# Performance work log

Measured on AMD Instinct MI355X. Metric: run time of the kernel, lower is better.

## Reference

```python
import jax, jax.numpy as jnp
import numpy as np
import math

HIDDEN = 1024
HEADS = 16
LAYERS = 4
IN_DIM = 512
OUT_DIM = 1024
B, S = 4, 2048


def _pos_encoding(seq_len, dim):
    pos = jnp.arange(seq_len, dtype=jnp.float32)[:, None]            # [S,1]
    div = jnp.exp(jnp.arange(0, dim, 2, dtype=jnp.float32) * (-math.log(10000.0) / dim))  # [D/2]
    ang = pos * div                                                   # [S,D/2]
    # interleave: even idx sin, odd idx cos
    return jnp.stack([jnp.sin(ang), jnp.cos(ang)], axis=-1).reshape(seq_len, dim)


def _layernorm(x, g, b, eps=1e-5):
    mu = jnp.mean(x, axis=-1, keepdims=True)
    var = jnp.var(x, axis=-1, keepdims=True)
    return (x - mu) * jax.lax.rsqrt(var + eps) * g + b


def setup_inputs() -> dict:
    key = jax.random.key(0)
    ks = jax.random.split(key, 8)
    d = {
        'x': jax.random.normal(ks[0], (B, S, IN_DIM), jnp.float32),
        'in_W': jax.random.normal(ks[1], (IN_DIM, HIDDEN), jnp.float32) * (1.0 / math.sqrt(IN_DIM)),
        'in_b': jnp.zeros((HIDDEN,), jnp.float32),
        'qkv_W': jax.random.normal(ks[2], (LAYERS, HIDDEN, 3 * HIDDEN), jnp.float32) * (1.0 / math.sqrt(HIDDEN)),
        'qkv_b': jnp.zeros((LAYERS, 3 * HIDDEN), jnp.float32),
        'out_W': jax.random.normal(ks[3], (LAYERS, HIDDEN, HIDDEN), jnp.float32) * (1.0 / math.sqrt(HIDDEN)),
        'out_b': jnp.zeros((LAYERS, HIDDEN), jnp.float32),
        'ln1_g': jnp.ones((LAYERS, HIDDEN), jnp.float32),
        'ln1_b': jnp.zeros((LAYERS, HIDDEN), jnp.float32),
        'ln2_g': jnp.ones((LAYERS, HIDDEN), jnp.float32),
        'ln2_b': jnp.zeros((LAYERS, HIDDEN), jnp.float32),
        'ff1_W': jax.random.normal(ks[4], (LAYERS, HIDDEN, 4 * HIDDEN), jnp.float32) * (1.0 / math.sqrt(HIDDEN)),
        'ff1_b': jnp.zeros((LAYERS, 4 * HIDDEN), jnp.float32),
        'ff2_W': jax.random.normal(ks[5], (LAYERS, 4 * HIDDEN, HIDDEN), jnp.float32) * (1.0 / math.sqrt(4 * HIDDEN)),
        'ff2_b': jnp.zeros((LAYERS, HIDDEN), jnp.float32),
        'fin_g': jnp.ones((HIDDEN,), jnp.float32),
        'fin_b': jnp.zeros((HIDDEN,), jnp.float32),
        'op_W': jax.random.normal(ks[6], (HIDDEN, OUT_DIM), jnp.float32) * (1.0 / math.sqrt(HIDDEN)),
        'op_b': jnp.zeros((OUT_DIM,), jnp.float32),
    }
    return d


def reference(x, in_W, in_b, qkv_W, qkv_b, out_W, out_b, ln1_g, ln1_b, ln2_g, ln2_b,
              ff1_W, ff1_b, ff2_W, ff2_b, fin_g, fin_b, op_W, op_b):
    b, s, _ = x.shape
    dh = HIDDEN // HEADS
    h = x @ in_W + in_b                                   # [B,S,D]
    h = h * math.sqrt(HIDDEN) + _pos_encoding(s, HIDDEN)  # scaled + PE (dropout=eval)
    for i in range(LAYERS):
        qkv = (h @ qkv_W[i] + qkv_b[i]).reshape(b, s, 3, HEADS, dh)
        q, k, v = qkv[:, :, 0], qkv[:, :, 1], qkv[:, :, 2]
        scores = jnp.einsum('bqhd,bkhd->bhqk', q, k) / math.sqrt(dh)
        attn = jax.nn.softmax(scores, axis=-1)
        ctx = jnp.einsum('bhqk,bkhd->bqhd', attn, v).reshape(b, s, HIDDEN)
        h = _layernorm(h + (ctx @ out_W[i] + out_b[i]), ln1_g[i], ln1_b[i])
        ff = jax.nn.relu(h @ ff1_W[i] + ff1_b[i]) @ ff2_W[i] + ff2_b[i]
        h = _layernorm(h + ff, ln2_g[i], ln2_b[i])
    h = _layernorm(h, fin_g, fin_b)
    return h @ op_W + op_b
```

## Files before the change

kernel.cpp:

```cpp
#include <hip/hip_runtime.h>
#include <math.h>

typedef unsigned short u16;
typedef __attribute__((ext_vector_type(8))) __bf16 bf16x8;
typedef __attribute__((ext_vector_type(4))) float floatx4;
typedef unsigned int __attribute__((address_space(1))) g_u32;
typedef unsigned int __attribute__((address_space(3))) l_u32;

#define EPI_BIAS  1
#define EPI_RELU  2
#define EPI_EMBED 8

__device__ __forceinline__ float bf2f(u16 u) {
    union { unsigned int i; float f; } v; v.i = ((unsigned int)u) << 16; return v.f;
}
__device__ __forceinline__ u16 f2bf(float f) {
    union { __bf16 b; u16 u; } v; v.b = (__bf16)f; return v.u;
}
__device__ __forceinline__ void gl_lds16(const void* g, void* l) {
    __builtin_amdgcn_global_load_lds((const g_u32*)g, (l_u32*)l, 16, 0, 0);
}
__device__ __forceinline__ float posenc(int s, int c) {
    double e = exp((double)(c & 1022) * (-9.210340371976184 / 1024.0));
    double ang = (double)s * e;
    return (float)((c & 1) ? cos(ang) : sin(ang));
}

template<bool SPLIT>
__global__ __launch_bounds__(256) void transpose_f2b(
    const float* __restrict__ in, u16* __restrict__ oh, u16* __restrict__ ol,
    int R, int C) {
    __shared__ float tile[32][33];
    int bx = blockIdx.x * 32, by = blockIdx.y * 32;
    int tx = threadIdx.x & 31, ty = threadIdx.x >> 5;
    #pragma unroll
    for (int i = ty; i < 32; i += 8) tile[i][tx] = in[(size_t)(by + i) * C + bx + tx];
    __syncthreads();
    #pragma unroll
    for (int i = ty; i < 32; i += 8) {
        float f = tile[tx][i];
        u16 hi = f2bf(f);
        oh[(size_t)(bx + i) * R + by + tx] = hi;
        if (SPLIT) ol[(size_t)(bx + i) * R + by + tx] = f2bf(f - bf2f(hi));
    }
}

template<int AMODE, int EPI, bool ACCUM, bool WF, bool WB>
__global__ __launch_bounds__(256) void gemm_k(
    const void* __restrict__ Ap, const u16* __restrict__ Bt,
    const float* __restrict__ bias,
    float* __restrict__ outF, u16* __restrict__ outB,
    int M, int N, int K) {
    __shared__ alignas(16) u16 As[128 * 32];
    __shared__ alignas(16) u16 Bs[128 * 32];
    const int tid = threadIdx.x;
    const int wave = tid >> 6, lane = tid & 63;
    const int l16 = lane & 15, quad = lane >> 4;
    const int bm = blockIdx.x * 128, bn = blockIdx.y * 128;
    const int wm = (wave & 1) * 64, wn = (wave >> 1) * 64;
    const int sr = tid >> 2, sc = (tid & 3) * 8;

    const u16* Abf = (const u16*)Ap;
    const float* Af = (const float*)Ap;

    floatx4 acc[4][4];
    floatx4 zero = {0.0f, 0.0f, 0.0f, 0.0f};
    #pragma unroll
    for (int i = 0; i < 4; ++i)
        #pragma unroll
        for (int j = 0; j < 4; ++j) acc[i][j] = zero;

    for (int k0 = 0; k0 < K; k0 += 32) {
        if (AMODE == 0) {
            #pragma unroll
            for (int p = 0; p < 2; ++p) {
                const u16* g = Abf + (size_t)(bm + sr + 64 * p) * K + k0 + sc;
                gl_lds16(g, &As[(p * 64 + (wave << 4)) * 32]);
            }
        } else {
            #pragma unroll
            for (int p = 0; p < 2; ++p) {
                const float* g = Af + (size_t)(bm + sr + 64 * p) * K + k0 + sc;
                union { u16 u[8]; uint4 v; } tmp;
                #pragma unroll
                for (int j = 0; j < 8; ++j) {
                    float f = g[j];
                    u16 h = f2bf(f);
                    if (AMODE == 2) h = f2bf(f - bf2f(h));
                    tmp.u[j] = h;
                }
                *(uint4*)&As[(sr + 64 * p) * 32 + sc] = tmp.v;
            }
        }
        #pragma unroll
        for (int p = 0; p < 2; ++p) {
            const u16* g = Bt + (size_t)(bn + sr + 64 * p) * K + k0 + sc;
            gl_lds16(g, &Bs[(p * 64 + (wave << 4)) * 32]);
        }
        __syncthreads();
        bf16x8 af[4], bfr[4];
        #pragma unroll
        for (int i = 0; i < 4; ++i) af[i] = *(const bf16x8*)&As[(wm + i * 16 + l16) * 32 + quad * 8];
        #pragma unroll
        for (int j = 0; j < 4; ++j) bfr[j] = *(const bf16x8*)&Bs[(wn + j * 16 + l16) * 32 + quad * 8];
        #pragma unroll
        for (int i = 0; i < 4; ++i)
            #pragma unroll
            for (int j = 0; j < 4; ++j)
                acc[i][j] = __builtin_amdgcn_mfma_f32_16x16x32_bf16(af[i], bfr[j], acc[i][j], 0, 0, 0);
        __syncthreads();
    }

    #pragma unroll
    for (int i = 0; i < 4; ++i) {
        #pragma unroll
        for (int r = 0; r < 4; ++r) {
            int row = bm + wm + i * 16 + quad * 4 + r;
            #pragma unroll
            for (int j = 0; j < 4; ++j) {
                int col = bn + wn + j * 16 + l16;
                float v = acc[i][j][r];
                if (EPI & EPI_BIAS) v += bias[col];
                if (ACCUM) v += outF[(size_t)row * N + col];
                if (EPI & EPI_EMBED) { v = v * 32.0f + posenc(row & 2047, col); }
                if (EPI & EPI_RELU) v = fmaxf(v, 0.0f);
                if (WF) outF[(size_t)row * N + col] = v;
                if (WB) outB[(size_t)row * N + col] = f2bf(v);
            }
        }
    }
}

__global__ __launch_bounds__(256) void attn_k(
    const float* __restrict__ qkv, u16* __restrict__ ctx) {
    constexpr int KSTR = 72;
    constexpr int VSTR = 72;
    constexpr int PSTR = 88;
    __shared__ alignas(16) u16 Kh[2][64 * KSTR];
    __shared__ alignas(16) u16 Kl[2][64 * KSTR];
    __shared__ alignas(16) u16 Vt[2][64 * VSTR];
    __shared__ alignas(16) u16 Ps[128 * PSTR];

    const int tid = threadIdx.x, wave = tid >> 6, lane = tid & 63;
    const int l16 = lane & 15, quad = lane >> 4;
    const int bh = blockIdx.x >> 4, qt = blockIdx.x & 15;
    const int b = bh >> 4, h = bh & 15;
    const size_t base = (size_t)b * 2048 * 3072;
    const int wq = wave * 32;

    const int kr = tid >> 2, kcb = (tid & 3) * 16;
    const float* gK = qkv + base + (size_t)kr * 3072 + 1024 + h * 64 + kcb;
    const int vk = lane, vdg = wave * 16;
    const float* gV = qkv + base + (size_t)vk * 3072 + 2048 + h * 64 + vdg;

    bf16x8 qh[2][2], ql[2][2];
    #pragma unroll
    for (int i = 0; i < 2; ++i) {
        const float* g = qkv + base + (size_t)(qt * 128 + wq + i * 16 + l16) * 3072 + h * 64 + quad * 8;
        #pragma unroll
        for (int kk = 0; kk < 2; ++kk) {
            float4 va = ((const float4*)(g + kk * 32))[0];
            float4 vb = ((const float4*)(g + kk * 32))[1];
            float f[8] = {va.x, va.y, va.z, va.w, vb.x, vb.y, vb.z, vb.w};
            union { u16 u[8]; bf16x8 v; } th, tl;
            #pragma unroll
            for (int j = 0; j < 8; ++j) {
                float s = f[j] * 0.125f;
                u16 hi = f2bf(s);
                th.u[j] = hi;
                tl.u[j] = f2bf(s - bf2f(hi));
            }
            qh[i][kk] = th.v; ql[i][kk] = tl.v;
        }
    }

    float4 pk4[4], pv4[4];
    auto LOAD = [&](int c) {
        const float* g = gK + (size_t)(c * 64) * 3072;
        pk4[0] = ((const float4*)g)[0]; pk4[1] = ((const float4*)g)[1];
        pk4[2] = ((const float4*)g)[2]; pk4[3] = ((const float4*)g)[3];
        const float* g2 = gV + (size_t)(c * 64) * 3072;
        pv4[0] = ((const float4*)g2)[0]; pv4[1] = ((const float4*)g2)[1];
        pv4[2] = ((const float4*)g2)[2]; pv4[3] = ((const float4*)g2)[3];
    };
    auto STORE = [&](int bu) {
        const float* pf = (const float*)pk4;
        union { u16 u[8]; uint4 q; } h0, h1, s0, s1;
        #pragma unroll
        for (int j = 0; j < 8; ++j) {
            float a = pf[j], c2 = pf[8 + j];
            u16 ah = f2bf(a); h0.u[j] = ah; s0.u[j] = f2bf(a - bf2f(ah));
            u16 ch = f2bf(c2); h1.u[j] = ch; s1.u[j] = f2bf(c2 - bf2f(ch));
        }
        *(uint4*)&Kh[bu][kr * KSTR + kcb]     = h0.q;
        *(uint4*)&Kh[bu][kr * KSTR + kcb + 8] = h1.q;
        *(uint4*)&Kl[bu][kr * KSTR + kcb]     = s0.q;
        *(uint4*)&Kl[bu][kr * KSTR + kcb + 8] = s1.q;
        const float* vf = (const float*)pv4;
        #pragma unroll
        for (int j = 0; j < 16; ++j)
            Vt[bu][(vdg + j) * VSTR + vk] = f2bf(vf[j]);
    };

    floatx4 acc_o[2][4];
    float mrun[2][4], lrun[2][4];
    floatx4 zf = {0.0f, 0.0f, 0.0f, 0.0f};
    #pragma unroll
    for (int i = 0; i < 2; ++i)
        #pragma unroll
        for (int j = 0; j < 4; ++j) acc_o[i][j] = zf;
    #pragma unroll
    for (int i = 0; i < 2; ++i)
        #pragma unroll
        for (int r = 0; r < 4; ++r) { mrun[i][r] = -1e30f; lrun[i][r] = 0.0f; }

    LOAD(0); STORE(0); LOAD(1);
    __syncthreads();

    for (int c = 0; c < 32; ++c) {
        const int cur = c & 1;

        floatx4 acc_s[2][4];
        #pragma unroll
        for (int i = 0; i < 2; ++i)
            #pragma unroll
            for (int j = 0; j < 4; ++j) acc_s[i][j] = zf;
        #pragma unroll
        for (int kk = 0; kk < 2; ++kk) {
            bf16x8 kbh[4], kbl[4];
            #pragma unroll
            for (int j = 0; j < 4; ++j) {
                kbh[j] = *(const bf16x8*)&Kh[cur][(j * 16 + l16) * KSTR + kk * 32 + quad * 8];
                kbl[j] = *(const bf16x8*)&Kl[cur][(j * 16 + l16) * KSTR + kk * 32 + quad * 8];
            }
            #pragma unroll
            for (int i = 0; i < 2; ++i)
                #pragma unroll
                for (int j = 0; j < 4; ++j) {
                    acc_s[i][j] = __builtin_amdgcn_mfma_f32_16x16x32_bf16(qh[i][kk], kbh[j], acc_s[i][j], 0, 0, 0);
                    acc_s[i][j] = __builtin_amdgcn_mfma_f32_16x16x32_bf16(ql[i][kk], kbh[j], acc_s[i][j], 0, 0, 0);
                    acc_s[i][j] = __builtin_amdgcn_mfma_f32_16x16x32_bf16(qh[i][kk], kbl[j], acc_s[i][j], 0, 0, 0);
                }
        }

        #pragma unroll
        for (int i = 0; i < 2; ++i) {
            #pragma unroll
            for (int r = 0; r < 4; ++r) {
                float mx = fmaxf(fmaxf(acc_s[i][0][r], acc_s[i][1][r]),
                                 fmaxf(acc_s[i][2][r], acc_s[i][3][r]));
                #pragma unroll
                for (int off = 8; off; off >>= 1) mx = fmaxf(mx, __shfl_xor(mx, off));
                float nm = fmaxf(mrun[i][r], mx);
                float sc = __expf(mrun[i][r] - nm);
                mrun[i][r] = nm;
                float rs = 0.0f;
                #pragma unroll
                for (int j = 0; j < 4; ++j) {
                    float p = __expf(acc_s[i][j][r] - nm);
                    acc_s[i][j][r] = p;
                    rs += p;
                }
                #pragma unroll
                for (int off = 8; off; off >>= 1) rs += __shfl_xor(rs, off);
                lrun[i][r] = lrun[i][r] * sc + rs;
                #pragma unroll
                for (int jd = 0; jd < 4; ++jd) acc_o[i][jd][r] *= sc;
                #pragma unroll
                for (int j = 0; j < 4; ++j)
                    Ps[(wq + i * 16 + quad * 4 + r) * PSTR + j * 16 + l16] = f2bf(acc_s[i][j][r]);
            }
        }
        asm volatile("s_waitcnt lgkmcnt(0)" ::: "memory");

        #pragma unroll
        for (int kk = 0; kk < 2; ++kk) {
            bf16x8 pa[2], vb[4];
            #pragma unroll
            for (int i = 0; i < 2; ++i)
                pa[i] = *(const bf16x8*)&Ps[(wq + i * 16 + l16) * PSTR + kk * 32 + quad * 8];
            #pragma unroll
            for (int jd = 0; jd < 4; ++jd)
                vb[jd] = *(const bf16x8*)&Vt[cur][(jd * 16 + l16) * VSTR + kk * 32 + quad * 8];
            #pragma unroll
            for (int i = 0; i < 2; ++i)
                #pragma unroll
                for (int jd = 0; jd < 4; ++jd)
                    acc_o[i][jd] = __builtin_amdgcn_mfma_f32_16x16x32_bf16(pa[i], vb[jd], acc_o[i][jd], 0, 0, 0);
        }

        if (c + 1 < 32) STORE(cur ^ 1);
        __syncthreads();
        if (c + 2 < 32) LOAD(c + 2);
    }

    #pragma unroll
    for (int i = 0; i < 2; ++i) {
        #pragma unroll
        for (int r = 0; r < 4; ++r) {
            float inv = 1.0f / lrun[i][r];
            size_t ro = (size_t)(b * 2048 + qt * 128 + wq + i * 16 + quad * 4 + r) * 1024 + h * 64;
            #pragma unroll
            for (int jd = 0; jd < 4; ++jd)
                ctx[ro + jd * 16 + l16] = f2bf(acc_o[i][jd][r] * inv);
        }
    }
}

__global__ __launch_bounds__(256) void ln_k(
    float* __restrict__ h, const float* __restrict__ g, const float* __restrict__ bb) {
    const int row = blockIdx.x, tid = threadIdx.x;
    const int wave = tid >> 6, lane = tid & 63;
    float4 v = *(const float4*)(h + (size_t)row * 1024 + tid * 4);
    float x[4] = {v.x, v.y, v.z, v.w};
    float s = x[0] + x[1] + x[2] + x[3];
    float s2 = x[0] * x[0] + x[1] * x[1] + x[2] * x[2] + x[3] * x[3];
    for (int off = 32; off; off >>= 1) { s += __shfl_xor(s, off); s2 += __shfl_xor(s2, off); }
    __shared__ float red[8];
    if (lane == 0) { red[wave] = s; red[4 + wave] = s2; }
    __syncthreads();
    s = red[0] + red[1] + red[2] + red[3];
    s2 = red[4] + red[5] + red[6] + red[7];
    float mu = s * (1.0f / 1024.0f);
    float var = s2 * (1.0f / 1024.0f) - mu * mu;
    float rs = rsqrtf(var + 1e-5f);
    float4 gg = *(const float4*)(g + tid * 4);
    float4 bp = *(const float4*)(bb + tid * 4);
    float4 o;
    o.x = (x[0] - mu) * rs * gg.x + bp.x;
    o.y = (x[1] - mu) * rs * gg.y + bp.y;
    o.z = (x[2] - mu) * rs * gg.z + bp.z;
    o.w = (x[3] - mu) * rs * gg.w + bp.w;
    *(float4*)(h + (size_t)row * 1024 + tid * 4) = o;
}

extern "C" void kernel_launch(void* const* d_in, const int* in_sizes, int n_in,
                              void* d_out, int out_size, void* d_ws, size_t ws_size,
                              hipStream_t stream) {
    const float* x     = (const float*)d_in[0];
    const float* in_W  = (const float*)d_in[1];
    const float* in_b  = (const float*)d_in[2];
    const float* qkv_W = (const float*)d_in[3];
    const float* qkv_b = (const float*)d_in[4];
    const float* out_W = (const float*)d_in[5];
    const float* out_b = (const float*)d_in[6];
    const float* ln1_g = (const float*)d_in[7];
    const float* ln1_b = (const float*)d_in[8];
    const float* ln2_g = (const float*)d_in[9];
    const float* ln2_b = (const float*)d_in[10];
    const float* ff1_W = (const float*)d_in[11];
    const float* ff1_b = (const float*)d_in[12];
    const float* ff2_W = (const float*)d_in[13];
    const float* ff2_b = (const float*)d_in[14];
    const float* fin_g = (const float*)d_in[15];
    const float* fin_b = (const float*)d_in[16];
    const float* op_W  = (const float*)d_in[17];
    const float* op_b  = (const float*)d_in[18];

    size_t off = 0;
    char* wsb = (char*)d_ws;
    auto alloc = [&](size_t bytes) { void* p = wsb + off; off += (bytes + 255) & ~(size_t)255; return p; };
    u16*   BtH  = (u16*)alloc((size_t)4096 * 1024 * 2);
    u16*   BtL  = (u16*)alloc((size_t)3072 * 1024 * 2);
    float* hbuf = (float*)alloc((size_t)8192 * 1024 * 4);
    float* qkvb = (float*)alloc((size_t)8192 * 3072 * 4);
    u16*   ctxb = (u16*)alloc((size_t)8192 * 1024 * 2);
    if (off > ws_size) return;

    dim3 tb(256);

    transpose_f2b<true><<<dim3(32, 16), tb, 0, stream>>>(in_W, BtH, BtL, 512, 1024);
    gemm_k<1, 0, false, true, false><<<dim3(64, 8), tb, 0, stream>>>(
        x, BtH, nullptr, hbuf, nullptr, 8192, 1024, 512);
    gemm_k<1, 0, true, true, false><<<dim3(64, 8), tb, 0, stream>>>(
        x, BtL, nullptr, hbuf, nullptr, 8192, 1024, 512);
    gemm_k<2, EPI_BIAS | EPI_EMBED, true, true, false><<<dim3(64, 8), tb, 0, stream>>>(
        x, BtH, in_b, hbuf, nullptr, 8192, 1024, 512);

    for (int L = 0; L < 4; ++L) {
        if (L == 0) {
            transpose_f2b<true><<<dim3(96, 32), tb, 0, stream>>>(
                qkv_W, BtH, BtL, 1024, 3072);
            gemm_k<1, 0, false, true, false><<<dim3(64, 24), tb, 0, stream>>>(
                hbuf, BtH, nullptr, qkvb, nullptr, 8192, 3072, 1024);
            gemm_k<1, 0, true, true, false><<<dim3(64, 24), tb, 0, stream>>>(
                hbuf, BtL, nullptr, qkvb, nullptr, 8192, 3072, 1024);
            gemm_k<2, EPI_BIAS, true, true, false><<<dim3(64, 24), tb, 0, stream>>>(
                hbuf, BtH, qkv_b, qkvb, nullptr, 8192, 3072, 1024);
        } else {
            transpose_f2b<false><<<dim3(96, 32), tb, 0, stream>>>(
                qkv_W + (size_t)L * 1024 * 3072, BtH, nullptr, 1024, 3072);
            gemm_k<1, EPI_BIAS, false, true, false><<<dim3(64, 24), tb, 0, stream>>>(
                hbuf, BtH, qkv_b + (size_t)L * 3072, qkvb, nullptr, 8192, 3072, 1024);
        }
        attn_k<<<dim3(1024), tb, 0, stream>>>(qkvb, ctxb);
        transpose_f2b<false><<<dim3(32, 32), tb, 0, stream>>>(
            out_W + (size_t)L * 1024 * 1024, BtH, nullptr, 1024, 1024);
        gemm_k<0, EPI_BIAS, true, true, false><<<dim3(64, 8), tb, 0, stream>>>(
            ctxb, BtH, out_b + (size_t)L * 1024, hbuf, nullptr, 8192, 1024, 1024);
        ln_k<<<8192, tb, 0, stream>>>(hbuf, ln1_g + (size_t)L * 1024, ln1_b + (size_t)L * 1024);
        transpose_f2b<false><<<dim3(128, 32), tb, 0, stream>>>(
            ff1_W + (size_t)L * 1024 * 4096, BtH, nullptr, 1024, 4096);
        gemm_k<1, EPI_BIAS | EPI_RELU, false, false, true><<<dim3(64, 32), tb, 0, stream>>>(
            hbuf, BtH, ff1_b + (size_t)L * 4096, nullptr, (u16*)qkvb, 8192, 4096, 1024);
        transpose_f2b<false><<<dim3(32, 128), tb, 0, stream>>>(
            ff2_W + (size_t)L * 4096 * 1024, BtH, nullptr, 4096, 1024);
        gemm_k<0, EPI_BIAS, true, true, false><<<dim3(64, 8), tb, 0, stream>>>(
            (u16*)qkvb, BtH, ff2_b + (size_t)L * 1024, hbuf, nullptr, 8192, 1024, 4096);
        ln_k<<<8192, tb, 0, stream>>>(hbuf, ln2_g + (size_t)L * 1024, ln2_b + (size_t)L * 1024);
    }

    ln_k<<<8192, tb, 0, stream>>>(hbuf, fin_g, fin_b);
    transpose_f2b<false><<<dim3(32, 32), tb, 0, stream>>>(op_W, BtH, nullptr, 1024, 1024);
    gemm_k<1, EPI_BIAS, false, true, false><<<dim3(64, 8), tb, 0, stream>>>(
        hbuf, BtH, op_b, (float*)d_out, nullptr, 8192, 1024, 1024);
}
```

Measured before the change: 3.212 ms.

## Pre-convert activations to bf16, drop split-precision attention after layer zero

Activations are now converted to bf16 (and hi/lo split) once, in a pre-pass, in layernorm, or in the embedding epilogue, so every GEMM loads A straight through global-to-LDS instead of converting fp32 on the fly. Attention keeps the three-product split-bf16 QK^T only in layer 0 and uses a single bf16 product in later layers. It also adds lazy online-softmax rescaling (rescale only when the running max grows by more than 8) and sets MFMA priority hints. These cut conversion work and MFMA count, at the cost of some precision and extra bf16 buffers.

```diff
diff --git a/kernel.cpp b/kernel.cpp
--- a/kernel.cpp
+++ b/kernel.cpp
@@ -26,9 +26,25 @@
     return (float)((c & 1) ? cos(ang) : sin(ang));
 }
 
-template<bool SPLIT>
+__global__ __launch_bounds__(256) void conv_split(
+    const float* __restrict__ in, u16* __restrict__ oh, u16* __restrict__ ol) {
+    const int i = (blockIdx.x * 256 + threadIdx.x) * 8;
+    float4 a = ((const float4*)(in + i))[0];
+    float4 b = ((const float4*)(in + i))[1];
+    float f[8] = {a.x, a.y, a.z, a.w, b.x, b.y, b.z, b.w};
+    union { u16 u[8]; uint4 q; } H, L;
+    #pragma unroll
+    for (int j = 0; j < 8; ++j) {
+        u16 hi = f2bf(f[j]);
+        H.u[j] = hi; L.u[j] = f2bf(f[j] - bf2f(hi));
+    }
+    *(uint4*)&oh[i] = H.q;
+    *(uint4*)&ol[i] = L.q;
+}
+
+template<int TMODE>
 __global__ __launch_bounds__(256) void transpose_f2b(
-    const float* __restrict__ in, u16* __restrict__ oh, u16* __restrict__ ol,
+    const float* __restrict__ in, u16* __restrict__ oh,
     int R, int C) {
     __shared__ float tile[32][33];
     int bx = blockIdx.x * 32, by = blockIdx.y * 32;
@@ -40,16 +56,16 @@
     for (int i = ty; i < 32; i += 8) {
         float f = tile[tx][i];
         u16 hi = f2bf(f);
-        oh[(size_t)(bx + i) * R + by + tx] = hi;
-        if (SPLIT) ol[(size_t)(bx + i) * R + by + tx] = f2bf(f - bf2f(hi));
-    }
-}
-
-template<int AMODE, int EPI, bool ACCUM, bool WF, bool WB>
+        u16 o = (TMODE == 2) ? f2bf(f - bf2f(hi)) : hi;
+        oh[(size_t)(bx + i) * R + by + tx] = o;
+    }
+}
+
+template<int EPI, bool ACCUM, bool WF, bool WB, bool WB2>
 __global__ __launch_bounds__(256) void gemm_k(
-    const void* __restrict__ Ap, const u16* __restrict__ Bt,
+    const u16* __restrict__ A, const u16* __restrict__ Bt,
     const float* __restrict__ bias,
-    float* __restrict__ outF, u16* __restrict__ outB,
+    float* __restrict__ outF, u16* __restrict__ outB, u16* __restrict__ outB2,
     int M, int N, int K) {
     __shared__ alignas(16) u16 As[128 * 32];
     __shared__ alignas(16) u16 Bs[128 * 32];
@@ -60,9 +76,6 @@
     const int wm = (wave & 1) * 64, wn = (wave >> 1) * 64;
     const int sr = tid >> 2, sc = (tid & 3) * 8;
 
-    const u16* Abf = (const u16*)Ap;
-    const float* Af = (const float*)Ap;
-
     floatx4 acc[4][4];
     floatx4 zero = {0.0f, 0.0f, 0.0f, 0.0f};
     #pragma unroll
@@ -71,31 +84,15 @@
         for (int j = 0; j < 4; ++j) acc[i][j] = zero;
 
     for (int k0 = 0; k0 < K; k0 += 32) {
-        if (AMODE == 0) {
-            #pragma unroll
-            for (int p = 0; p < 2; ++p) {
-                const u16* g = Abf + (size_t)(bm + sr + 64 * p) * K + k0 + sc;
-                gl_lds16(g, &As[(p * 64 + (wave << 4)) * 32]);
-            }
-        } else {
-            #pragma unroll
-            for (int p = 0; p < 2; ++p) {
-                const float* g = Af + (size_t)(bm + sr + 64 * p) * K + k0 + sc;
-                union { u16 u[8]; uint4 v; } tmp;
-                #pragma unroll
-                for (int j = 0; j < 8; ++j) {
-                    float f = g[j];
-                    u16 h = f2bf(f);
-                    if (AMODE == 2) h = f2bf(f - bf2f(h));
-                    tmp.u[j] = h;
-                }
-                *(uint4*)&As[(sr + 64 * p) * 32 + sc] = tmp.v;
-            }
-        }
         #pragma unroll
         for (int p = 0; p < 2; ++p) {
-            const u16* g = Bt + (size_t)(bn + sr + 64 * p) * K + k0 + sc;
-            gl_lds16(g, &Bs[(p * 64 + (wave << 4)) * 32]);
+            const u16* ga = A + (size_t)(bm + sr + 64 * p) * K + k0 + sc;
+            gl_lds16(ga, &As[(p * 64 + (wave << 4)) * 32]);
+        }
+        #pragma unroll
+        for (int p = 0; p < 2; ++p) {
+            const u16* gb = Bt + (size_t)(bn + sr + 64 * p) * K + k0 + sc;
+            gl_lds16(gb, &Bs[(p * 64 + (wave << 4)) * 32]);
         }
         __syncthreads();
         bf16x8 af[4], bfr[4];
@@ -125,19 +122,24 @@
                 if (EPI & EPI_EMBED) { v = v * 32.0f + posenc(row & 2047, col); }
                 if (EPI & EPI_RELU) v = fmaxf(v, 0.0f);
                 if (WF) outF[(size_t)row * N + col] = v;
-                if (WB) outB[(size_t)row * N + col] = f2bf(v);
+                if (WB) {
+                    u16 hi = f2bf(v);
+                    outB[(size_t)row * N + col] = hi;
+                    if (WB2) outB2[(size_t)row * N + col] = f2bf(v - bf2f(hi));
+                }
             }
         }
     }
 }
 
+template<bool SPLIT>
 __global__ __launch_bounds__(256) void attn_k(
     const float* __restrict__ qkv, u16* __restrict__ ctx) {
     constexpr int KSTR = 72;
     constexpr int VSTR = 72;
     constexpr int PSTR = 88;
     __shared__ alignas(16) u16 Kh[2][64 * KSTR];
-    __shared__ alignas(16) u16 Kl[2][64 * KSTR];
+    __shared__ alignas(16) u16 Kl[2][SPLIT ? 64 * KSTR : 8];
     __shared__ alignas(16) u16 Vt[2][64 * VSTR];
     __shared__ alignas(16) u16 Ps[128 * PSTR];
 
@@ -168,9 +170,10 @@
                 float s = f[j] * 0.125f;
                 u16 hi = f2bf(s);
                 th.u[j] = hi;
-                tl.u[j] = f2bf(s - bf2f(hi));
+                if (SPLIT) tl.u[j] = f2bf(s - bf2f(hi));
             }
-            qh[i][kk] = th.v; ql[i][kk] = tl.v;
+            qh[i][kk] = th.v;
+            if (SPLIT) ql[i][kk] = tl.v;
         }
     }
 
@@ -189,13 +192,16 @@
         #pragma unroll
         for (int j = 0; j < 8; ++j) {
             float a = pf[j], c2 = pf[8 + j];
-            u16 ah = f2bf(a); h0.u[j] = ah; s0.u[j] = f2bf(a - bf2f(ah));
-            u16 ch = f2bf(c2); h1.u[j] = ch; s1.u[j] = f2bf(c2 - bf2f(ch));
+            u16 ah = f2bf(a); h0.u[j] = ah;
+            u16 ch = f2bf(c2); h1.u[j] = ch;
+            if (SPLIT) { s0.u[j] = f2bf(a - bf2f(ah)); s1.u[j] = f2bf(c2 - bf2f(ch)); }
         }
         *(uint4*)&Kh[bu][kr * KSTR + kcb]     = h0.q;
         *(uint4*)&Kh[bu][kr * KSTR + kcb + 8] = h1.q;
-        *(uint4*)&Kl[bu][kr * KSTR + kcb]     = s0.q;
-        *(uint4*)&Kl[bu][kr * KSTR + kcb + 8] = s1.q;
+        if (SPLIT) {
+            *(uint4*)&Kl[bu][kr * KSTR + kcb]     = s0.q;
+            *(uint4*)&Kl[bu][kr * KSTR + kcb + 8] = s1.q;
+        }
         const float* vf = (const float*)pv4;
         #pragma unroll
         for (int j = 0; j < 16; ++j)
@@ -231,46 +237,69 @@
             #pragma unroll
             for (int j = 0; j < 4; ++j) {
                 kbh[j] = *(const bf16x8*)&Kh[cur][(j * 16 + l16) * KSTR + kk * 32 + quad * 8];
-                kbl[j] = *(const bf16x8*)&Kl[cur][(j * 16 + l16) * KSTR + kk * 32 + quad * 8];
+                if (SPLIT) kbl[j] = *(const bf16x8*)&Kl[cur][(j * 16 + l16) * KSTR + kk * 32 + quad * 8];
             }
+            __builtin_amdgcn_s_setprio(1);
             #pragma unroll
             for (int i = 0; i < 2; ++i)
                 #pragma unroll
                 for (int j = 0; j < 4; ++j) {
                     acc_s[i][j] = __builtin_amdgcn_mfma_f32_16x16x32_bf16(qh[i][kk], kbh[j], acc_s[i][j], 0, 0, 0);
-                    acc_s[i][j] = __builtin_amdgcn_mfma_f32_16x16x32_bf16(ql[i][kk], kbh[j], acc_s[i][j], 0, 0, 0);
-                    acc_s[i][j] = __builtin_amdgcn_mfma_f32_16x16x32_bf16(qh[i][kk], kbl[j], acc_s[i][j], 0, 0, 0);
+                    if (SPLIT) {
+                        acc_s[i][j] = __builtin_amdgcn_mfma_f32_16x16x32_bf16(ql[i][kk], kbh[j], acc_s[i][j], 0, 0, 0);
+                        acc_s[i][j] = __builtin_amdgcn_mfma_f32_16x16x32_bf16(qh[i][kk], kbl[j], acc_s[i][j], 0, 0, 0);
+                    }
                 }
-        }
-
-        #pragma unroll
-        for (int i = 0; i < 2; ++i) {
+            __builtin_amdgcn_s_setprio(0);
+        }
+
+        float mx[2][4];
+        #pragma unroll
+        for (int i = 0; i < 2; ++i)
             #pragma unroll
             for (int r = 0; r < 4; ++r) {
-                float mx = fmaxf(fmaxf(acc_s[i][0][r], acc_s[i][1][r]),
+                float m0 = fmaxf(fmaxf(acc_s[i][0][r], acc_s[i][1][r]),
                                  fmaxf(acc_s[i][2][r], acc_s[i][3][r]));
                 #pragma unroll
-                for (int off = 8; off; off >>= 1) mx = fmaxf(mx, __shfl_xor(mx, off));
-                float nm = fmaxf(mrun[i][r], mx);
-                float sc = __expf(mrun[i][r] - nm);
-                mrun[i][r] = nm;
+                for (int off = 8; off; off >>= 1) m0 = fmaxf(m0, __shfl_xor(m0, off));
+                mx[i][r] = m0;
+            }
+        bool up = false;
+        #pragma unroll
+        for (int i = 0; i < 2; ++i)
+            #pragma unroll
+            for (int r = 0; r < 4; ++r) up = up || (mx[i][r] > mrun[i][r] + 8.0f);
+        if (__any(up)) {
+            #pragma unroll
+            for (int i = 0; i < 2; ++i)
+                #pragma unroll
+                for (int r = 0; r < 4; ++r) {
+                    float nm = fmaxf(mrun[i][r], mx[i][r]);
+                    float sc = __expf(mrun[i][r] - nm);
+                    mrun[i][r] = nm;
+                    lrun[i][r] *= sc;
+                    #pragma unroll
+                    for (int jd = 0; jd < 4; ++jd) acc_o[i][jd][r] *= sc;
+                }
+        }
+        #pragma unroll
+        for (int i = 0; i < 2; ++i)
+            #pragma unroll
+            for (int r = 0; r < 4; ++r) {
                 float rs = 0.0f;
                 #pragma unroll
                 for (int j = 0; j < 4; ++j) {
-                    float p = __expf(acc_s[i][j][r] - nm);
+                    float p = __expf(acc_s[i][j][r] - mrun[i][r]);
                     acc_s[i][j][r] = p;
                     rs += p;
                 }
                 #pragma unroll
                 for (int off = 8; off; off >>= 1) rs += __shfl_xor(rs, off);
-                lrun[i][r] = lrun[i][r] * sc + rs;
-                #pragma unroll
-                for (int jd = 0; jd < 4; ++jd) acc_o[i][jd][r] *= sc;
+                lrun[i][r] += rs;
                 #pragma unroll
                 for (int j = 0; j < 4; ++j)
                     Ps[(wq + i * 16 + quad * 4 + r) * PSTR + j * 16 + l16] = f2bf(acc_s[i][j][r]);
             }
-        }
         asm volatile("s_waitcnt lgkmcnt(0)" ::: "memory");
 
         #pragma unroll
@@ -282,11 +311,13 @@
             #pragma unroll
             for (int jd = 0; jd < 4; ++jd)
                 vb[jd] = *(const bf16x8*)&Vt[cur][(jd * 16 + l16) * VSTR + kk * 32 + quad * 8];
+            __builtin_amdgcn_s_setprio(1);
             #pragma unroll
             for (int i = 0; i < 2; ++i)
                 #pragma unroll
                 for (int jd = 0; jd < 4; ++jd)
                     acc_o[i][jd] = __builtin_amdgcn_mfma_f32_16x16x32_bf16(pa[i], vb[jd], acc_o[i][jd], 0, 0, 0);
+            __builtin_amdgcn_s_setprio(0);
         }
 
         if (c + 1 < 32) STORE(cur ^ 1);
@@ -308,7 +339,8 @@
 }
 
 __global__ __launch_bounds__(256) void ln_k(
-    float* __restrict__ h, const float* __restrict__ g, const float* __restrict__ bb) {
+    float* __restrict__ h, const float* __restrict__ g, const float* __restrict__ bb,
+    u16* __restrict__ hb) {
     const int row = blockIdx.x, tid = threadIdx.x;
     const int wave = tid >> 6, lane = tid & 63;
     float4 v = *(const float4*)(h + (size_t)row * 1024 + tid * 4);
@@ -332,6 +364,10 @@
     o.z = (x[2] - mu) * rs * gg.z + bp.z;
     o.w = (x[3] - mu) * rs * gg.w + bp.w;
     *(float4*)(h + (size_t)row * 1024 + tid * 4) = o;
+    union { u16 u[4]; uint2 q; } hb4;
+    hb4.u[0] = f2bf(o.x); hb4.u[1] = f2bf(o.y);
+    hb4.u[2] = f2bf(o.z); hb4.u[3] = f2bf(o.w);
+    *(uint2*)&hb[(size_t)row * 1024 + tid * 4] = hb4.q;
 }
 
 extern "C" void kernel_launch(void* const* d_in, const int* in_sizes, int n_in,
@@ -361,57 +397,65 @@
     char* wsb = (char*)d_ws;
     auto alloc = [&](size_t bytes) { void* p = wsb + off; off += (bytes + 255) & ~(size_t)255; return p; };
     u16*   BtH  = (u16*)alloc((size_t)4096 * 1024 * 2);
-    u16*   BtL  = (u16*)alloc((size_t)3072 * 1024 * 2);
     float* hbuf = (float*)alloc((size_t)8192 * 1024 * 4);
     float* qkvb = (float*)alloc((size_t)8192 * 3072 * 4);
     u16*   ctxb = (u16*)alloc((size_t)8192 * 1024 * 2);
+    u16*   hbfH = (u16*)alloc((size_t)8192 * 1024 * 2);
     if (off > ws_size) return;
+    u16* xh  = (u16*)qkvb;
+    u16* xl  = xh + (size_t)8192 * 512;
+    u16* h0h = ctxb;
+    u16* h0l = hbfH;
+    u16* ffb = (u16*)qkvb;
 
     dim3 tb(256);
 
-    transpose_f2b<true><<<dim3(32, 16), tb, 0, stream>>>(in_W, BtH, BtL, 512, 1024);
-    gemm_k<1, 0, false, true, false><<<dim3(64, 8), tb, 0, stream>>>(
-        x, BtH, nullptr, hbuf, nullptr, 8192, 1024, 512);
-    gemm_k<1, 0, true, true, false><<<dim3(64, 8), tb, 0, stream>>>(
-        x, BtL, nullptr, hbuf, nullptr, 8192, 1024, 512);
-    gemm_k<2, EPI_BIAS | EPI_EMBED, true, true, false><<<dim3(64, 8), tb, 0, stream>>>(
-        x, BtH, in_b, hbuf, nullptr, 8192, 1024, 512);
+    conv_split<<<dim3(2048), tb, 0, stream>>>(x, xh, xl);
+    transpose_f2b<0><<<dim3(32, 16), tb, 0, stream>>>(in_W, BtH, 512, 1024);
+    gemm_k<0, false, true, false, false><<<dim3(64, 8), tb, 0, stream>>>(
+        xh, BtH, nullptr, hbuf, nullptr, nullptr, 8192, 1024, 512);
+    gemm_k<0, true, true, false, false><<<dim3(64, 8), tb, 0, stream>>>(
+        xl, BtH, nullptr, hbuf, nullptr, nullptr, 8192, 1024, 512);
+    transpose_f2b<2><<<dim3(32, 16), tb, 0, stream>>>(in_W, BtH, 512, 1024);
+    gemm_k<EPI_BIAS | EPI_EMBED, true, true, true, true><<<dim3(64, 8), tb, 0, stream>>>(
+        xh, BtH, in_b, hbuf, h0h, h0l, 8192, 1024, 512);
 
     for (int L = 0; L < 4; ++L) {
         if (L == 0) {
-            transpose_f2b<true><<<dim3(96, 32), tb, 0, stream>>>(
-                qkv_W, BtH, BtL, 1024, 3072);
-            gemm_k<1, 0, false, true, false><<<dim3(64, 24), tb, 0, stream>>>(
-                hbuf, BtH, nullptr, qkvb, nullptr, 8192, 3072, 1024);
-            gemm_k<1, 0, true, true, false><<<dim3(64, 24), tb, 0, stream>>>(
-                hbuf, BtL, nullptr, qkvb, nullptr, 8192, 3072, 1024);
-            gemm_k<2, EPI_BIAS, true, true, false><<<dim3(64, 24), tb, 0, stream>>>(
-                hbuf, BtH, qkv_b, qkvb, nullptr, 8192, 3072, 1024);
+            transpose_f2b<0><<<dim3(96, 32), tb, 0, stream>>>(qkv_W, BtH, 1024, 3072);
+            gemm_k<0, false, true, false, false><<<dim3(64, 24), tb, 0, stream>>>(
+                h0h, BtH, nullptr, qkvb, nullptr, nullptr, 8192, 3072, 1024);
+            gemm_k<0, true, true, false, false><<<dim3(64, 24), tb, 0, stream>>>(
+                h0l, BtH, nullptr, qkvb, nullptr, nullptr, 8192, 3072, 1024);
+            transpose_f2b<2><<<dim3(96, 32), tb, 0, stream>>>(qkv_W, BtH, 1024, 3072);
+            gemm_k<EPI_BIAS, true, true, false, false><<<dim3(64, 24), tb, 0, stream>>>(
+                h0h, BtH, qkv_b, qkvb, nullptr, nullptr, 8192, 3072, 1024);
         } else {
-            transpose_f2b<false><<<dim3(96, 32), tb, 0, stream>>>(
-                qkv_W + (size_t)L * 1024 * 3072, BtH, nullptr, 1024, 3072);
-            gemm_k<1, EPI_BIAS, false, true, false><<<dim3(64, 24), tb, 0, stream>>>(
-                hbuf, BtH, qkv_b + (size_t)L * 3072, qkvb, nullptr, 8192, 3072, 1024);
-        }
-        attn_k<<<dim3(1024), tb, 0, stream>>>(qkvb, ctxb);
-        transpose_f2b<false><<<dim3(32, 32), tb, 0, stream>>>(
-            out_W + (size_t)L * 1024 * 1024, BtH, nullptr, 1024, 1024);
-        gemm_k<0, EPI_BIAS, true, true, false><<<dim3(64, 8), tb, 0, stream>>>(
-            ctxb, BtH, out_b + (size_t)L * 1024, hbuf, nullptr, 8192, 1024, 1024);
-        ln_k<<<8192, tb, 0, stream>>>(hbuf, ln1_g + (size_t)L * 1024, ln1_b + (size_t)L * 1024);
-        transpose_f2b<false><<<dim3(128, 32), tb, 0, stream>>>(
-            ff1_W + (size_t)L * 1024 * 4096, BtH, nullptr, 1024, 4096);
-        gemm_k<1, EPI_BIAS | EPI_RELU, false, false, true><<<dim3(64, 32), tb, 0, stream>>>(
-            hbuf, BtH, ff1_b + (size_t)L * 4096, nullptr, (u16*)qkvb, 8192, 4096, 1024);
-        transpose_f2b<false><<<dim3(32, 128), tb, 0, stream>>>(
-            ff2_W + (size_t)L * 4096 * 1024, BtH, nullptr, 4096, 1024);
-        gemm_k<0, EPI_BIAS, true, true, false><<<dim3(64, 8), tb, 0, stream>>>(
-            (u16*)qkvb, BtH, ff2_b + (size_t)L * 1024, hbuf, nullptr, 8192, 1024, 4096);
-        ln_k<<<8192, tb, 0, stream>>>(hbuf, ln2_g + (size_t)L * 1024, ln2_b + (size_t)L * 1024);
-    }
-
-    ln_k<<<8192, tb, 0, stream>>>(hbuf, fin_g, fin_b);
-    transpose_f2b<false><<<dim3(32, 32), tb, 0, stream>>>(op_W, BtH, nullptr, 1024, 1024);
-    gemm_k<1, EPI_BIAS, false, true, false><<<dim3(64, 8), tb, 0, stream>>>(
-        hbuf, BtH, op_b, (float*)d_out, nullptr, 8192, 1024, 1024);
-}
+            transpose_f2b<0><<<dim3(96, 32), tb, 0, stream>>>(
+                qkv_W + (size_t)L * 1024 * 3072, BtH, 1024, 3072);
+            gemm_k<EPI_BIAS, false, true, false, false><<<dim3(64, 24), tb, 0, stream>>>(
+                hbfH, BtH, qkv_b + (size_t)L * 3072, qkvb, nullptr, nullptr, 8192, 3072, 1024);
+        }
+        if (L == 0) attn_k<true><<<dim3(1024), tb, 0, stream>>>(qkvb, ctxb);
+        else        attn_k<false><<<dim3(1024), tb, 0, stream>>>(qkvb, ctxb);
+        transpose_f2b<0><<<dim3(32, 32), tb, 0, stream>>>(
+            out_W + (size_t)L * 1024 * 1024, BtH, 1024, 1024);
+        gemm_k<EPI_BIAS, true, true, false, false><<<dim3(64, 8), tb, 0, stream>>>(
+            ctxb, BtH, out_b + (size_t)L * 1024, hbuf, nullptr, nullptr, 8192, 1024, 1024);
+        ln_k<<<8192, tb, 0, stream>>>(hbuf, ln1_g + (size_t)L * 1024, ln1_b + (size_t)L * 1024, hbfH);
+        transpose_f2b<0><<<dim3(128, 32), tb, 0, stream>>>(
+            ff1_W + (size_t)L * 1024 * 4096, BtH, 1024, 4096);
+        gemm_k<EPI_BIAS | EPI_RELU, false, false, true, false><<<dim3(64, 32), tb, 0, stream>>>(
+            hbfH, BtH, ff1_b + (size_t)L * 4096, nullptr, ffb, nullptr, 8192, 4096, 1024);
+        transpose_f2b<0><<<dim3(32, 128), tb, 0, stream>>>(
+            ff2_W + (size_t)L * 4096 * 1024, BtH, 4096, 1024);
+        gemm_k<EPI_BIAS, true, true, false, false><<<dim3(64, 8), tb, 0, stream>>>(
+            ffb, BtH, ff2_b + (size_t)L * 1024, hbuf, nullptr, nullptr, 8192, 1024, 4096);
+        ln_k<<<8192, tb, 0, stream>>>(hbuf, ln2_g + (size_t)L * 1024, ln2_b + (size_t)L * 1024, hbfH);
+    }
+
+    ln_k<<<8192, tb, 0, stream>>>(hbuf, fin_g, fin_b, hbfH);
+    transpose_f2b<0><<<dim3(32, 32), tb, 0, stream>>>(op_W, BtH, 1024, 1024);
+    gemm_k<EPI_BIAS, false, true, false, false><<<dim3(64, 8), tb, 0, stream>>>(
+        hbfH, BtH, op_b, (float*)d_out, nullptr, nullptr, 8192, 1024, 1024);
+}
```

Measured after the change: 2.937 ms. -8.6%, faster.
